# Kernel optimization log

Hardware: AMD Instinct MI355X
Metric: run time of the kernel (lower is better)

The kernel has to match this reference:

```python
import jax, jax.numpy as jnp
import numpy as np

B, N, IN_CH = 4, 8192, 4
K = 16
W0, W1, W2 = 64, 128, 256
NUM_CLASSES = 3


def setup_inputs() -> dict:
    key = jax.random.key(0)
    ks = jax.random.split(key, 16)

    def lin(kw, kb, fan_in, fan_out):
        bound = 1.0 / np.sqrt(fan_in)
        w = jax.random.uniform(kw, (fan_in, fan_out), jnp.float32, -bound, bound)
        b = jax.random.uniform(kb, (fan_out,), jnp.float32, -bound, bound)
        return w, b

    x = jax.random.normal(ks[0], (B, N, IN_CH), jnp.float32)
    stem_w, stem_b = lin(ks[1], ks[2], IN_CH, W0)
    b1_w, b1_b = lin(ks[3], ks[4], 2 * W0 + 3, W1)
    b2_w, b2_b = lin(ks[5], ks[6], 2 * W1 + 3, W2)
    glob_w, glob_b = lin(ks[7], ks[8], W2, W2)
    head1_w, head1_b = lin(ks[9], ks[10], 2 * W2, W2)
    head2_w, head2_b = lin(ks[11], ks[12], W2, NUM_CLASSES)
    return {
        'x': x,
        'hmix_a': jnp.float32(1.0), 'hmix_b': jnp.float32(1.0), 'hmix_c': jnp.float32(0.0),
        'stem_w': stem_w, 'stem_b': stem_b,
        'b1_w': b1_w, 'b1_b': b1_b,
        'b2_w': b2_w, 'b2_b': b2_b,
        'glob_w': glob_w, 'glob_b': glob_b,
        'head1_w': head1_w, 'head1_b': head1_b,
        'head2_w': head2_w, 'head2_b': head2_b,
        'thresh': jnp.float32(0.15), 'sharp': jnp.float32(10.0), 'scale': jnp.float32(0.5),
    }


def _knn_idx(coords, k):
    # coords: [B,N,3] -> idx of k nearest neighbors (incl. self), no grad.
    c = jax.lax.stop_gradient(coords)
    xx = jnp.sum(c * c, axis=-1, keepdims=True)            # [B,N,1]
    dist = xx + jnp.swapaxes(xx, 1, 2) - 2.0 * jnp.einsum('bnc,bmc->bnm', c, c)
    dist = jnp.maximum(dist, 0.0)
    _, idx = jax.lax.top_k(-dist, k)                       # smallest distances
    return idx                                             # [B,N,k]


def _local_agg(coords, feat, idx, w, b):
    # gather-concat-MLP-maxpool, faithful to LocalAggBlock (pool='max')
    bidx = jnp.arange(coords.shape[0])[:, None, None]
    nb_f = feat[bidx, idx]                                 # [B,N,k,C]
    nb_p = coords[bidx, idx]                               # [B,N,k,3]
    fi = feat[:, :, None, :]
    pi = coords[:, :, None, :]
    h = jnp.concatenate(
        [jnp.broadcast_to(fi, nb_f.shape), nb_f - fi, nb_p - pi], axis=-1)
    h = jax.nn.relu(jnp.einsum('bnkd,do->bnko', h, w) + b)
    return jnp.max(h, axis=2)                              # [B,N,out]


def reference(x, hmix_a, hmix_b, hmix_c, stem_w, stem_b, b1_w, b1_b,
              b2_w, b2_b, glob_w, glob_b, head1_w, head1_b,
              head2_w, head2_b, thresh, sharp, scale):
    # HeightMixer: z_eff = a*z + b*hag + c
    z_eff = hmix_a * x[..., 2] + hmix_b * x[..., 3] + hmix_c
    coords = jnp.stack([x[..., 0], x[..., 1], z_eff], axis=-1)  # [B,N,3]

    f = jax.nn.relu(x @ stem_w + stem_b)                   # stem: [B,N,64]

    # both blocks use the same coords -> same KNN graph; compute once
    idx = _knn_idx(coords, K)
    f = _local_agg(coords, f, idx, b1_w, b1_b)             # [B,N,128]
    f = _local_agg(coords, f, idx, b2_w, b2_b)             # [B,N,256]

    g = jnp.max(f, axis=1)                                 # [B,256]
    g = jax.nn.relu(g @ glob_w + glob_b)
    g = jnp.broadcast_to(g[:, None, :], f.shape)           # [B,N,256]

    h = jnp.concatenate([f, g], axis=-1)                   # [B,N,512]
    h = jax.nn.relu(h @ head1_w + head1_b)
    logits = h @ head2_w + head2_b                         # [B,N,3]

    # HeightPriorBias on class 0
    hag = x[..., 3]
    bias = scale * jax.nn.sigmoid(sharp * (thresh - hag))
    logits = logits.at[..., 0].add(bias)
    return logits
```

## Files before the change

kernel.cpp:

```cpp
#include <hip/hip_runtime.h>
#include <math.h>

typedef unsigned long long u64;
typedef unsigned int u32;
typedef _Float16 h8v __attribute__((ext_vector_type(8)));
typedef float    f4v __attribute__((ext_vector_type(4)));
typedef float    f2v __attribute__((ext_vector_type(2)));

#define MFMA16(a,b,c) __builtin_amdgcn_mfma_f32_16x16x32_f16(a, b, c, 0, 0, 0)

#define B_ 4
#define N_ 8192
#define K_ 16
#define W0_ 64
#define W1_ 128
#define W2_ 256
#define X0_ 96
#define X1_ 160
#define QAD_ 32
#define CAP_ 128

__global__ __launch_bounds__(256) void prep_kernel(
    const float* __restrict__ x,
    const float* __restrict__ stem_w, const float* __restrict__ stem_b,
    const float* __restrict__ hmix_a, const float* __restrict__ hmix_b,
    const float* __restrict__ hmix_c,
    float* __restrict__ coords4, _Float16* __restrict__ fx0,
    _Float16* __restrict__ fx1,
    const float* __restrict__ b1_w, const float* __restrict__ b2_w,
    const float* __restrict__ h1w,
    _Float16* __restrict__ w1m, _Float16* __restrict__ w1d,
    _Float16* __restrict__ w2m, _Float16* __restrict__ w2d,
    _Float16* __restrict__ h1wT,
    _Float16* __restrict__ qa, _Float16* __restrict__ cbq,
    float* __restrict__ part) {
  const int bi = blockIdx.x;
  const int tid = threadIdx.x;
  const int PB = (B_*N_)/4;
  if (bi < PB) {
    const int p = bi * 4 + (tid >> 6);
    const int o = tid & 63;
    const float x0 = x[p*4+0], x1 = x[p*4+1], x2 = x[p*4+2], x3 = x[p*4+3];
    const float z = hmix_a[0]*x2 + hmix_b[0]*x3 + hmix_c[0];
    float acc = stem_b[o] + x0*stem_w[0*W0_+o] + x1*stem_w[1*W0_+o]
              + x2*stem_w[2*W0_+o] + x3*stem_w[3*W0_+o];
    fx0[p*X0_+o] = (_Float16)fmaxf(acc, 0.f);
    if (o < 32) {
      const float tv = (o==0) ? x0 : (o==1) ? x1 : (o==2) ? z : 0.f;
      fx0[p*X0_+W0_+o] = (_Float16)tv;
      fx1[(size_t)p*X1_+W1_+o] = (_Float16)tv;
    }
    if (o == 0) {
      const float xx = x0*x0 + x1*x1 + z*z;
      ((float4*)coords4)[p] = make_float4(x0, x1, z, xx);
    } else if (o == 1) {
      const _Float16 hx = (_Float16)x0, hy = (_Float16)x1, hz = (_Float16)z;
      const _Float16 lx = (_Float16)(x0 - (float)hx);
      const _Float16 ly = (_Float16)(x1 - (float)hy);
      const _Float16 lz = (_Float16)(z  - (float)hz);
      const _Float16 one = (_Float16)1.f, Z = (_Float16)0.f;
      h8v a0 = {hx, hy, hz, lx, ly, lz, hx, hy};
      h8v a1 = {hz, lx, ly, lz, one, one, Z, Z};
      h8v zr = {Z,Z,Z,Z,Z,Z,Z,Z};
      *(h8v*)(qa + (size_t)p*QAD_)      = a0;
      *(h8v*)(qa + (size_t)p*QAD_ + 8)  = a1;
      *(h8v*)(qa + (size_t)p*QAD_ + 16) = zr;
      *(h8v*)(qa + (size_t)p*QAD_ + 24) = zr;
    } else if (o == 2) {
      const _Float16 hx = (_Float16)x0, hy = (_Float16)x1, hz = (_Float16)z;
      const _Float16 lx = (_Float16)(x0 - (float)hx);
      const _Float16 ly = (_Float16)(x1 - (float)hy);
      const _Float16 lz = (_Float16)(z  - (float)hz);
      const float xx = x0*x0 + x1*x1 + z*z;
      const _Float16 xh = (_Float16)xx;
      const _Float16 xl = (_Float16)(xx - (float)xh);
      const _Float16 nhx = (_Float16)(-2.f*(float)hx);
      const _Float16 nhy = (_Float16)(-2.f*(float)hy);
      const _Float16 nhz = (_Float16)(-2.f*(float)hz);
      const _Float16 nlx = (_Float16)(-2.f*(float)lx);
      const _Float16 nly = (_Float16)(-2.f*(float)ly);
      const _Float16 nlz = (_Float16)(-2.f*(float)lz);
      const _Float16 Z = (_Float16)0.f;
      h8v b0 = {nhx, nhy, nhz, nlx, nly, nlz, nlx, nly};
      h8v b1 = {nlz, nhx, nhy, nhz, xh, xl, Z, Z};
      h8v zr = {Z,Z,Z,Z,Z,Z,Z,Z};
      *(h8v*)(cbq + (size_t)p*QAD_)      = b0;
      *(h8v*)(cbq + (size_t)p*QAD_ + 8)  = b1;
      *(h8v*)(cbq + (size_t)p*QAD_ + 16) = zr;
      *(h8v*)(cbq + (size_t)p*QAD_ + 24) = zr;
    }
  } else if (bi < PB + W1_) {
    const int o = bi - PB, c = tid;
    if (c < X0_) {
      float mv = 0.f, dv = 0.f;
      if (c < W0_)        { const float wm = b1_w[(W0_+c)*W1_+o]; mv = wm; dv = b1_w[c*W1_+o] - wm; }
      else if (c < W0_+3) { const float wp = b1_w[(2*W0_+(c-W0_))*W1_+o]; mv = wp; dv = -wp; }
      w1m[o*X0_+c] = (_Float16)mv;
      w1d[o*X0_+c] = (_Float16)dv;
    }
  } else if (bi < PB + W1_ + W2_) {
    const int o = bi - PB - W1_, c = tid;
    if (c < X1_) {
      float mv = 0.f, dv = 0.f;
      if (c < W1_)        { const float wm = b2_w[(W1_+c)*W2_+o]; mv = wm; dv = b2_w[c*W2_+o] - wm; }
      else if (c < W1_+3) { const float wp = b2_w[(2*W1_+(c-W1_))*W2_+o]; mv = wp; dv = -wp; }
      w2m[o*X1_+c] = (_Float16)mv;
      w2d[o*X1_+c] = (_Float16)dv;
    }
  } else if (bi < PB + W1_ + 2*W2_) {
    const int o = bi - PB - W1_ - W2_;
    for (int c = tid; c < 512; c += 256)
      h1wT[(size_t)o*512 + c] = (_Float16)h1w[(size_t)c*256 + o];
  } else {
    ((float4*)part)[tid] = make_float4(0.f, 0.f, 0.f, 0.f);
  }
}

#define DPP_MIN(v, ctrl)                                                        \
  { const int _t = __builtin_amdgcn_update_dpp(0, __float_as_int(v),            \
      ctrl, 0xF, 0xF, false);                                                   \
    v = fminf(v, __int_as_float(_t)); }

__device__ __forceinline__ float sixteenth_of_minima(float v) {
  float th = 0.f;
#pragma unroll
  for (int r = 0; r < 16; ++r) {
    float w = v;
    DPP_MIN(w, 0x111); DPP_MIN(w, 0x112); DPP_MIN(w, 0x114); DPP_MIN(w, 0x118);
    DPP_MIN(w, 0x142); DPP_MIN(w, 0x143);
    const float mv = __int_as_float(
        __builtin_amdgcn_readlane(__float_as_int(w), 63));
    th = mv;
    v = (v == mv) ? INFINITY : v;
  }
  return th;
}

#define KNN_DIST2(dA, dB)                                                       \
  const f2v cjx = {cj.x, cj.x}, cjy = {cj.y, cj.y},                             \
            cjz = {cj.z, cj.z}, cjw = {cj.w, cj.w};                             \
  f2v tA = cAx * cjx;                                                           \
  tA = __builtin_elementwise_fma(cAy, cjy, tA);                                 \
  tA = __builtin_elementwise_fma(cAz, cjz, tA);                                 \
  const f2v dA = __builtin_elementwise_fma(tA, m2, cAw + cjw);                  \
  f2v tB = cBx * cjx;                                                           \
  tB = __builtin_elementwise_fma(cBy, cjy, tB);                                 \
  tB = __builtin_elementwise_fma(cBz, cjz, tB);                                 \
  const f2v dB = __builtin_elementwise_fma(tB, m2, cBw + cjw);

__global__ __launch_bounds__(256, 4) void knn_kernel(
    const float* __restrict__ coords4, const _Float16* __restrict__ qa,
    const _Float16* __restrict__ cbq, int* __restrict__ knn_idx) {
  const int tid = threadIdx.x;
  const int wid = tid >> 6;
  const int lane = tid & 63;
  const int col = lane & 15, quad = lane >> 4;
  const int p0 = blockIdx.x * 16;
  const int bb = (p0 >> 13) << 13;

  __shared__ float s_Tp[16];
  __shared__ int   s_cnt[16];
  __shared__ float s_ld[16][CAP_];
  __shared__ int   s_li[16][CAP_];
  if (tid < 16) s_cnt[tid] = 0;

  const float4* cb = ((const float4*)coords4) + bb;
  const int q0 = p0 + wid * 4;
  const float4 c0 = ((const float4*)coords4)[q0+0];
  const float4 c1 = ((const float4*)coords4)[q0+1];
  const float4 c2 = ((const float4*)coords4)[q0+2];
  const float4 c3 = ((const float4*)coords4)[q0+3];
  const f2v m2 = {-2.f, -2.f};
  const f2v cAx = {c0.x, c1.x}, cAy = {c0.y, c1.y}, cAz = {c0.z, c1.z}, cAw = {c0.w, c1.w};
  const f2v cBx = {c2.x, c3.x}, cBy = {c2.y, c3.y}, cBz = {c2.z, c3.z}, cBw = {c2.w, c3.w};

  float lm0 = INFINITY, lm1 = INFINITY, lm2 = INFINITY, lm3 = INFINITY;
  for (int it = 0; it < 64; ++it) {
    const float4 cj = cb[it*64 + lane];
    KNN_DIST2(dA, dB)
    lm0 = fminf(lm0, fmaxf(dA[0], 0.f));
    lm1 = fminf(lm1, fmaxf(dA[1], 0.f));
    lm2 = fminf(lm2, fmaxf(dB[0], 0.f));
    lm3 = fminf(lm3, fmaxf(dB[1], 0.f));
  }
  const float Th0 = sixteenth_of_minima(lm0);
  const float Th1 = sixteenth_of_minima(lm1);
  const float Th2 = sixteenth_of_minima(lm2);
  const float Th3 = sixteenth_of_minima(lm3);
  if (lane == 0) {
    s_Tp[wid*4+0] = Th0 - c0.w + (1e-3f + 1e-5f*c0.w);
    s_Tp[wid*4+1] = Th1 - c1.w + (1e-3f + 1e-5f*c1.w);
    s_Tp[wid*4+2] = Th2 - c2.w + (1e-3f + 1e-5f*c2.w);
    s_Tp[wid*4+3] = Th3 - c3.w + (1e-3f + 1e-5f*c3.w);
  }
  __syncthreads();

  const float Tq0 = s_Tp[quad*4+0], Tq1 = s_Tp[quad*4+1],
              Tq2 = s_Tp[quad*4+2], Tq3 = s_Tp[quad*4+3];
  const h8v afrag = *(const h8v*)(qa + (size_t)(p0 + col)*QAD_ + quad*8);
  const int cb0 = wid * 2048;
  const _Float16* cbp = cbq + (size_t)(bb + cb0 + col)*QAD_ + quad*8;

  h8v bcur = *(const h8v*)cbp;
#pragma unroll 2
  for (int t = 0; t < 128; ++t) {
    const int nx = ((t < 127) ? (t+1) : 0) * 16 * QAD_;
    const h8v bnxt = *(const h8v*)(cbp + nx);
    f4v acc = {0.f, 0.f, 0.f, 0.f};
    acc = MFMA16(afrag, bcur, acc);
    const int cidx = cb0 + t*16 + col;
    if (acc[0] < Tq0) { const int pos = atomicAdd(&s_cnt[quad*4+0], 1);
      if (pos < CAP_) { s_ld[quad*4+0][pos] = acc[0]; s_li[quad*4+0][pos] = cidx; } }
    if (acc[1] < Tq1) { const int pos = atomicAdd(&s_cnt[quad*4+1], 1);
      if (pos < CAP_) { s_ld[quad*4+1][pos] = acc[1]; s_li[quad*4+1][pos] = cidx; } }
    if (acc[2] < Tq2) { const int pos = atomicAdd(&s_cnt[quad*4+2], 1);
      if (pos < CAP_) { s_ld[quad*4+2][pos] = acc[2]; s_li[quad*4+2][pos] = cidx; } }
    if (acc[3] < Tq3) { const int pos = atomicAdd(&s_cnt[quad*4+3], 1);
      if (pos < CAP_) { s_ld[quad*4+3][pos] = acc[3]; s_li[quad*4+3][pos] = cidx; } }
    bcur = bnxt;
  }
  __syncthreads();

  for (int qq = 0; qq < 4; ++qq) {
    const int q = wid*4 + qq;
    const int cnt = s_cnt[q];
    const int L = (cnt < CAP_) ? cnt : CAP_;
    float d0 = (lane      < L) ? s_ld[q][lane]      : INFINITY;
    float d1 = (lane + 64 < L) ? s_ld[q][lane + 64] : INFINITY;
    int   i0 = (lane      < L) ? s_li[q][lane]      : 0x7fffffff;
    int   i1 = (lane + 64 < L) ? s_li[q][lane + 64] : 0x7fffffff;
    int keep = 0;
    for (int r = 0; r < K_; ++r) {
      float dl = d0; int il = i0; bool s1 = false;
      if (d1 < dl || (d1 == dl && i1 < il)) { dl = d1; il = i1; s1 = true; }
      float w = dl;
      DPP_MIN(w, 0x111); DPP_MIN(w, 0x112); DPP_MIN(w, 0x114); DPP_MIN(w, 0x118);
      DPP_MIN(w, 0x142); DPP_MIN(w, 0x143);
      const float dmin = __int_as_float(
          __builtin_amdgcn_readlane(__float_as_int(w), 63));
      u64 m = __ballot(dl == dmin);
      int bi = 0x7fffffff, bl = 0;
      do {
        const int s = (int)__ffsll((unsigned long long)m) - 1; m &= m - 1;
        const int ii = __builtin_amdgcn_readlane(il, s);
        if (ii < bi) { bi = ii; bl = s; }
      } while (m);
      if (lane == bl) { if (s1) d1 = INFINITY; else d0 = INFINITY; }
      if (lane == r) keep = bi;
    }
    if (lane < K_) knn_idx[(size_t)(p0 + q)*K_ + lane] = keep;
  }
}

template<int KS, int NPASS, bool GMAX>
__global__ __launch_bounds__(256) void aggm_kernel(
    const _Float16* __restrict__ fx, const int* __restrict__ knn_idx,
    const _Float16* __restrict__ midT, const _Float16* __restrict__ difT,
    const float* __restrict__ bw,
    _Float16* __restrict__ fo, const int ostr, u32* __restrict__ part) {
  const int XD  = KS*32;
  const int XDP = XD + 8;
  const int CH  = KS*4;
  const int p0 = blockIdx.x * 16;
  const int bb = (p0 >> 13) << 13;
  const int tid = threadIdx.x;
  const int w = tid >> 6, lane = tid & 63, col = lane & 15, quad = lane >> 4;
  const int koff = quad * 8;

  __shared__ int s_idx[256];
  __shared__ _Float16 sA[2][64*(KS*32+8)];

  s_idx[tid] = knn_idx[p0*K_ + tid];

  f4v cacc[NPASS][2];
  {
    h8v Ao[KS];
    const _Float16* ap = fx + (size_t)(p0+col)*XD + koff;
#pragma unroll
    for (int kk = 0; kk < KS; ++kk) Ao[kk] = *(const h8v*)(ap + kk*32);
#pragma unroll
    for (int ps = 0; ps < NPASS; ++ps) {
      const int o0 = ps*128 + w*32;
      const _Float16* b0 = difT + (size_t)(o0 + col)*XD + koff;
      const _Float16* b1 = difT + (size_t)(o0 + 16 + col)*XD + koff;
      f4v c0 = {0.f,0.f,0.f,0.f}, c1 = {0.f,0.f,0.f,0.f};
#pragma unroll
      for (int kk = 0; kk < KS; ++kk) {
        c0 = MFMA16(Ao[kk], *(const h8v*)(b0 + kk*32), c0);
        c1 = MFMA16(Ao[kk], *(const h8v*)(b1 + kk*32), c1);
      }
      cacc[ps][0] = c0; cacc[ps][1] = c1;
    }
  }

  h8v Bf[NPASS][2][KS];
  float bias[NPASS][2];
#pragma unroll
  for (int ps = 0; ps < NPASS; ++ps) {
    const int o0 = ps*128 + w*32;
#pragma unroll
    for (int kk = 0; kk < KS; ++kk) {
      Bf[ps][0][kk] = *(const h8v*)(midT + (size_t)(o0 + col)*XD + kk*32 + koff);
      Bf[ps][1][kk] = *(const h8v*)(midT + (size_t)(o0 + 16 + col)*XD + kk*32 + koff);
    }
    bias[ps][0] = bw[o0 + col];
    bias[ps][1] = bw[o0 + 16 + col];
  }
  __syncthreads();

  for (int c = tid; c < 64*CH; c += 256) {
    const int r = c / CH, o = c - r*CH;
    *(uint4*)&sA[0][r*XDP + o*8] =
        *(const uint4*)(fx + (size_t)(bb + s_idx[((r&15)<<4) + (r>>4)])*XD + o*8);
  }
  __syncthreads();

  f4v M[NPASS][2];
#pragma unroll
  for (int ps = 0; ps < NPASS; ++ps) {
    M[ps][0] = (f4v){-INFINITY,-INFINITY,-INFINITY,-INFINITY};
    M[ps][1] = (f4v){-INFINITY,-INFINITY,-INFINITY,-INFINITY};
  }

  for (int s = 0; s < 4; ++s) {
    const int buf = s & 1;
    if (s < 3) {
      for (int c = tid; c < 64*CH; c += 256) {
        const int r = c / CH, o = c - r*CH;
        *(uint4*)&sA[buf^1][r*XDP + o*8] =
            *(const uint4*)(fx + (size_t)(bb + s_idx[((r&15)<<4) + 4*s+4 + (r>>4)])*XD + o*8);
      }
    }
#pragma unroll
    for (int half = 0; half < 4; ++half) {
      h8v Ac[KS];
      const _Float16* ap = &sA[buf][(half*16 + col)*XDP + koff];
#pragma unroll
      for (int kk = 0; kk < KS; ++kk) Ac[kk] = *(const h8v*)(ap + kk*32);
#pragma unroll
      for (int ps = 0; ps < NPASS; ++ps) {
        f4v d0 = {0.f,0.f,0.f,0.f}, d1 = {0.f,0.f,0.f,0.f};
#pragma unroll
        for (int kk = 0; kk < KS; ++kk) {
          d0 = MFMA16(Ac[kk], Bf[ps][0][kk], d0);
          d1 = MFMA16(Ac[kk], Bf[ps][1][kk], d1);
        }
#pragma unroll
        for (int e = 0; e < 4; ++e) {
          M[ps][0][e] = fmaxf(M[ps][0][e], d0[e]);
          M[ps][1][e] = fmaxf(M[ps][1][e], d1[e]);
        }
      }
    }
    if (s < 3) __syncthreads();
  }

  const int prow = p0 + (quad << 2);
  const int bq = p0 >> 13;
#pragma unroll
  for (int ps = 0; ps < NPASS; ++ps) {
    const int o0 = ps*128 + w*32;
    const int oa = o0 + col, ob = oa + 16;
    float v0[4], v1[4];
#pragma unroll
    for (int reg = 0; reg < 4; ++reg) {
      v0[reg] = fmaxf(M[ps][0][reg] + cacc[ps][0][reg] + bias[ps][0], 0.f);
      v1[reg] = fmaxf(M[ps][1][reg] + cacc[ps][1][reg] + bias[ps][1], 0.f);
      fo[(size_t)(prow+reg)*ostr + oa] = (_Float16)v0[reg];
      fo[(size_t)(prow+reg)*ostr + ob] = (_Float16)v1[reg];
    }
    if (GMAX) {
      float bm0 = fmaxf(fmaxf(v0[0], v0[1]), fmaxf(v0[2], v0[3]));
      float bm1 = fmaxf(fmaxf(v1[0], v1[1]), fmaxf(v1[2], v1[3]));
      bm0 = fmaxf(bm0, __shfl_xor(bm0, 16, 64));
      bm0 = fmaxf(bm0, __shfl_xor(bm0, 32, 64));
      bm1 = fmaxf(bm1, __shfl_xor(bm1, 16, 64));
      bm1 = fmaxf(bm1, __shfl_xor(bm1, 32, 64));
      if (quad == 0) {
        atomicMax(part + bq*W2_ + oa, __float_as_uint(bm0));
        atomicMax(part + bq*W2_ + ob, __float_as_uint(bm1));
      }
    }
  }
}

__global__ __launch_bounds__(256) void gfc_kernel(
    const float* __restrict__ part, const float* __restrict__ gw,
    const float* __restrict__ gb, _Float16* __restrict__ g2h) {
  const int b = blockIdx.x;
  const int o = threadIdx.x;
  __shared__ float s_g[W2_];
  s_g[o] = part[b*W2_ + o];
  __syncthreads();
  float acc = gb[o];
  for (int d = 0; d < W2_; ++d) acc += s_g[d]*gw[d*W2_ + o];
  g2h[b*W2_ + o] = (_Float16)fmaxf(acc, 0.f);
}

__global__ __launch_bounds__(256) void headm_kernel(
    const _Float16* __restrict__ f2h, const _Float16* __restrict__ g2h,
    const _Float16* __restrict__ h1wT, const float* __restrict__ h1b,
    const float* __restrict__ h2w, const float* __restrict__ h2b,
    const float* __restrict__ x,
    const float* __restrict__ thresh, const float* __restrict__ sharp,
    const float* __restrict__ scale,
    float* __restrict__ out) {
  const int p0 = blockIdx.x * 32;
  const int b = p0 >> 13;
  const int tid = threadIdx.x;
  const int w = tid >> 6, lane = tid & 63, col = lane & 15, quad = lane >> 4;

  __shared__ _Float16 sA[32*520];
  __shared__ float    sh[32*260];

  for (int t = tid; t < 32*32; t += 256) {
    const int r = t >> 5, cc = (t & 31) * 8;
    *(uint4*)&sA[r*520 + cc] = *(const uint4*)&f2h[(size_t)(p0+r)*W2_ + cc];
  }
  for (int t = tid; t < 32*32; t += 256) {
    const int r = t >> 5, cc = (t & 31) * 8;
    *(uint4*)&sA[r*520 + 256 + cc] = *(const uint4*)&g2h[b*W2_ + cc];
  }
  __syncthreads();

  f4v acc[2][4];
#pragma unroll
  for (int r = 0; r < 2; ++r)
#pragma unroll
    for (int t = 0; t < 4; ++t) acc[r][t] = (f4v){0.f,0.f,0.f,0.f};

  for (int kk = 0; kk < 16; ++kk) {
    const h8v a0 = *(const h8v*)&sA[col*520 + kk*32 + quad*8];
    const h8v a1 = *(const h8v*)&sA[(16+col)*520 + kk*32 + quad*8];
#pragma unroll
    for (int t = 0; t < 4; ++t) {
      const h8v bt = *(const h8v*)&h1wT[(size_t)(w*64 + t*16 + col)*512 + kk*32 + quad*8];
      acc[0][t] = MFMA16(a0, bt, acc[0][t]);
      acc[1][t] = MFMA16(a1, bt, acc[1][t]);
    }
  }
#pragma unroll
  for (int r = 0; r < 2; ++r)
#pragma unroll
    for (int t = 0; t < 4; ++t) {
      const int o = w*64 + t*16 + col;
      const float bv = h1b[o];
#pragma unroll
      for (int reg = 0; reg < 4; ++reg)
        sh[(r*16 + quad*4 + reg)*260 + o] = fmaxf(acc[r][t][reg] + bv, 0.f);
    }
  __syncthreads();

  if (tid < 96) {
    const int pp = tid / 3, c = tid % 3;
    float s = h2b[c];
    for (int d = 0; d < 256; ++d) s += sh[pp*260 + d] * h2w[d*3 + c];
    if (c == 0) {
      const float hag = x[(size_t)(p0+pp)*4 + 3];
      s += scale[0] / (1.f + expf(-sharp[0]*(thresh[0] - hag)));
    }
    out[(size_t)(p0+pp)*3 + c] = s;
  }
}

extern "C" void kernel_launch(void* const* d_in, const int* in_sizes, int n_in,
                              void* d_out, int out_size, void* d_ws, size_t ws_size,
                              hipStream_t stream) {
  const float* x       = (const float*)d_in[0];
  const float* hmix_a  = (const float*)d_in[1];
  const float* hmix_b  = (const float*)d_in[2];
  const float* hmix_c  = (const float*)d_in[3];
  const float* stem_w  = (const float*)d_in[4];
  const float* stem_b  = (const float*)d_in[5];
  const float* b1_w    = (const float*)d_in[6];
  const float* b1_b    = (const float*)d_in[7];
  const float* b2_w    = (const float*)d_in[8];
  const float* b2_b    = (const float*)d_in[9];
  const float* glob_w  = (const float*)d_in[10];
  const float* glob_b  = (const float*)d_in[11];
  const float* head1_w = (const float*)d_in[12];
  const float* head1_b = (const float*)d_in[13];
  const float* head2_w = (const float*)d_in[14];
  const float* head2_b = (const float*)d_in[15];
  const float* thresh  = (const float*)d_in[16];
  const float* sharp   = (const float*)d_in[17];
  const float* scale   = (const float*)d_in[18];
  float* out = (float*)d_out;

  char* base = (char*)d_ws;
  float*     coords4 = (float*)    (base + 0);
  int*       idxb    = (int*)      (base + 524288);
  _Float16*  fx0     = (_Float16*) (base + 2621440);
  _Float16*  fx1     = (_Float16*) (base + 8912896);
  _Float16*  f2h     = (_Float16*) (base + 19398656);
  _Float16*  qa      = (_Float16*) (base + 19398656);
  _Float16*  cbq     = (_Float16*) (base + 21495808);
  _Float16*  w1m     = (_Float16*) (base + 36175872);
  _Float16*  w1d     = (_Float16*) (base + 36200448);
  _Float16*  w2m     = (_Float16*) (base + 36225024);
  _Float16*  w2d     = (_Float16*) (base + 36306944);
  _Float16*  h1wT    = (_Float16*) (base + 36388864);
  float*     part    = (float*)    (base + 36651008);
  _Float16*  g2h     = (_Float16*) (base + 36782080);
  const int NP = B_ * N_;

  prep_kernel<<<NP/4 + W1_ + 2*W2_ + 1, 256, 0, stream>>>(
      x, stem_w, stem_b, hmix_a, hmix_b, hmix_c, coords4, fx0, fx1,
      b1_w, b2_w, head1_w, w1m, w1d, w2m, w2d, h1wT, qa, cbq, part);
  knn_kernel<<<NP/16, 256, 0, stream>>>(coords4, qa, cbq, idxb);
  aggm_kernel<3, 1, false><<<NP/16, 256, 0, stream>>>(
      fx0, idxb, w1m, w1d, b1_b, fx1, X1_, (u32*)0);
  aggm_kernel<5, 2, true><<<NP/16, 256, 0, stream>>>(
      fx1, idxb, w2m, w2d, b2_b, f2h, W2_, (u32*)part);
  gfc_kernel<<<B_, 256, 0, stream>>>(part, glob_w, glob_b, g2h);
  headm_kernel<<<NP/32, 256, 0, stream>>>(f2h, g2h, h1wT, head1_b, head2_w, head2_b,
                                          x, thresh, sharp, scale, out);
}
```

Measured before the change: 394.6 us.

## Switch KNN distance pass to 32x32x16 MFMA with 32-query blocks

The KNN candidate-distance loop now uses the 32x32x16 f16 MFMA instead of 16x16x32, processing 32 queries per 512-thread block. The padded query and candidate rows shrink from 32 to 16 halves, since the extra K was all zeros. This halves the per-point fragment traffic and the number of MFMA issues per candidate. The cost is a larger accumulator per lane (16 thresholds and 16 compare/atomic branches), more shared memory, and a different block occupancy.

```diff
diff --git a/kernel.cpp b/kernel.cpp
--- a/kernel.cpp
+++ b/kernel.cpp
@@ -5,9 +5,11 @@
 typedef unsigned int u32;
 typedef _Float16 h8v __attribute__((ext_vector_type(8)));
 typedef float    f4v __attribute__((ext_vector_type(4)));
+typedef float    f16v __attribute__((ext_vector_type(16)));
 typedef float    f2v __attribute__((ext_vector_type(2)));
 
 #define MFMA16(a,b,c) __builtin_amdgcn_mfma_f32_16x16x32_f16(a, b, c, 0, 0, 0)
+#define MFMA32(a,b,c) __builtin_amdgcn_mfma_f32_32x32x16_f16(a, b, c, 0, 0, 0)
 
 #define B_ 4
 #define N_ 8192
@@ -17,7 +19,7 @@
 #define W2_ 256
 #define X0_ 96
 #define X1_ 160
-#define QAD_ 32
+#define QAD_ 16
 #define CAP_ 128
 
 __global__ __launch_bounds__(256) void prep_kernel(
@@ -61,11 +63,8 @@
       const _Float16 one = (_Float16)1.f, Z = (_Float16)0.f;
       h8v a0 = {hx, hy, hz, lx, ly, lz, hx, hy};
       h8v a1 = {hz, lx, ly, lz, one, one, Z, Z};
-      h8v zr = {Z,Z,Z,Z,Z,Z,Z,Z};
       *(h8v*)(qa + (size_t)p*QAD_)      = a0;
       *(h8v*)(qa + (size_t)p*QAD_ + 8)  = a1;
-      *(h8v*)(qa + (size_t)p*QAD_ + 16) = zr;
-      *(h8v*)(qa + (size_t)p*QAD_ + 24) = zr;
     } else if (o == 2) {
       const _Float16 hx = (_Float16)x0, hy = (_Float16)x1, hz = (_Float16)z;
       const _Float16 lx = (_Float16)(x0 - (float)hx);
@@ -83,11 +82,8 @@
       const _Float16 Z = (_Float16)0.f;
       h8v b0 = {nhx, nhy, nhz, nlx, nly, nlz, nlx, nly};
       h8v b1 = {nlz, nhx, nhy, nhz, xh, xl, Z, Z};
-      h8v zr = {Z,Z,Z,Z,Z,Z,Z,Z};
       *(h8v*)(cbq + (size_t)p*QAD_)      = b0;
       *(h8v*)(cbq + (size_t)p*QAD_ + 8)  = b1;
-      *(h8v*)(cbq + (size_t)p*QAD_ + 16) = zr;
-      *(h8v*)(cbq + (size_t)p*QAD_ + 24) = zr;
     }
   } else if (bi < PB + W1_) {
     const int o = bi - PB, c = tid;
@@ -148,21 +144,21 @@
   tB = __builtin_elementwise_fma(cBz, cjz, tB);                                 \
   const f2v dB = __builtin_elementwise_fma(tB, m2, cBw + cjw);
 
-__global__ __launch_bounds__(256, 4) void knn_kernel(
+__global__ __launch_bounds__(512) void knn_kernel(
     const float* __restrict__ coords4, const _Float16* __restrict__ qa,
     const _Float16* __restrict__ cbq, int* __restrict__ knn_idx) {
   const int tid = threadIdx.x;
   const int wid = tid >> 6;
   const int lane = tid & 63;
-  const int col = lane & 15, quad = lane >> 4;
-  const int p0 = blockIdx.x * 16;
+  const int p0 = blockIdx.x * 32;
   const int bb = (p0 >> 13) << 13;
 
-  __shared__ float s_Tp[16];
-  __shared__ int   s_cnt[16];
-  __shared__ float s_ld[16][CAP_];
-  __shared__ int   s_li[16][CAP_];
-  if (tid < 16) s_cnt[tid] = 0;
+  __shared__ float s_Tp[32];
+  __shared__ float s_Tpr[32];
+  __shared__ int   s_cnt[32];
+  __shared__ float s_ld[32][CAP_];
+  __shared__ int   s_li[32][CAP_];
+  if (tid < 32) s_cnt[tid] = 0;
 
   const float4* cb = ((const float4*)coords4) + bb;
   const int q0 = p0 + wid * 4;
@@ -194,29 +190,38 @@
     s_Tp[wid*4+3] = Th3 - c3.w + (1e-3f + 1e-5f*c3.w);
   }
   __syncthreads();
-
-  const float Tq0 = s_Tp[quad*4+0], Tq1 = s_Tp[quad*4+1],
-              Tq2 = s_Tp[quad*4+2], Tq3 = s_Tp[quad*4+3];
-  const h8v afrag = *(const h8v*)(qa + (size_t)(p0 + col)*QAD_ + quad*8);
-  const int cb0 = wid * 2048;
-  const _Float16* cbp = cbq + (size_t)(bb + cb0 + col)*QAD_ + quad*8;
+  if (tid < 32) {
+    const int h = tid >> 4, r = tid & 15;
+    s_Tpr[tid] = s_Tp[(r&3) + 8*(r>>2) + 4*h];
+  }
+  __syncthreads();
+
+  const int half = lane >> 5;
+  const int lrow = lane & 31;
+  float Tv[16];
+  *(f4v*)&Tv[0]  = *(const f4v*)&s_Tpr[half*16 + 0];
+  *(f4v*)&Tv[4]  = *(const f4v*)&s_Tpr[half*16 + 4];
+  *(f4v*)&Tv[8]  = *(const f4v*)&s_Tpr[half*16 + 8];
+  *(f4v*)&Tv[12] = *(const f4v*)&s_Tpr[half*16 + 12];
+  const h8v afrag = *(const h8v*)(qa + (size_t)(p0 + lrow)*QAD_ + half*8);
+  const int c0b = wid * 1024;
+  const _Float16* cbp = cbq + (size_t)(bb + c0b + lrow)*QAD_ + half*8;
+  const f16v zacc = (f16v)0.0f;
 
   h8v bcur = *(const h8v*)cbp;
 #pragma unroll 2
-  for (int t = 0; t < 128; ++t) {
-    const int nx = ((t < 127) ? (t+1) : 0) * 16 * QAD_;
-    const h8v bnxt = *(const h8v*)(cbp + nx);
-    f4v acc = {0.f, 0.f, 0.f, 0.f};
-    acc = MFMA16(afrag, bcur, acc);
-    const int cidx = cb0 + t*16 + col;
-    if (acc[0] < Tq0) { const int pos = atomicAdd(&s_cnt[quad*4+0], 1);
-      if (pos < CAP_) { s_ld[quad*4+0][pos] = acc[0]; s_li[quad*4+0][pos] = cidx; } }
-    if (acc[1] < Tq1) { const int pos = atomicAdd(&s_cnt[quad*4+1], 1);
-      if (pos < CAP_) { s_ld[quad*4+1][pos] = acc[1]; s_li[quad*4+1][pos] = cidx; } }
-    if (acc[2] < Tq2) { const int pos = atomicAdd(&s_cnt[quad*4+2], 1);
-      if (pos < CAP_) { s_ld[quad*4+2][pos] = acc[2]; s_li[quad*4+2][pos] = cidx; } }
-    if (acc[3] < Tq3) { const int pos = atomicAdd(&s_cnt[quad*4+3], 1);
-      if (pos < CAP_) { s_ld[quad*4+3][pos] = acc[3]; s_li[quad*4+3][pos] = cidx; } }
+  for (int t = 0; t < 32; ++t) {
+    const h8v bnxt = *(const h8v*)(cbp + (size_t)((t < 31) ? (t+1) : 0) * 32 * QAD_);
+    const f16v acc = MFMA32(afrag, bcur, zacc);
+    const int cidx = c0b + t*32 + lrow;
+#pragma unroll
+    for (int r = 0; r < 16; ++r) {
+      if (acc[r] < Tv[r]) {
+        const int q = (r&3) + 8*(r>>2) + 4*half;
+        const int pos = atomicAdd(&s_cnt[q], 1);
+        if (pos < CAP_) { s_ld[q][pos] = acc[r]; s_li[q][pos] = cidx; }
+      }
+    }
     bcur = bnxt;
   }
   __syncthreads();
@@ -494,7 +499,7 @@
   _Float16*  fx1     = (_Float16*) (base + 8912896);
   _Float16*  f2h     = (_Float16*) (base + 19398656);
   _Float16*  qa      = (_Float16*) (base + 19398656);
-  _Float16*  cbq     = (_Float16*) (base + 21495808);
+  _Float16*  cbq     = (_Float16*) (base + 20447232);
   _Float16*  w1m     = (_Float16*) (base + 36175872);
   _Float16*  w1d     = (_Float16*) (base + 36200448);
   _Float16*  w2m     = (_Float16*) (base + 36225024);
@@ -507,7 +512,7 @@
   prep_kernel<<<NP/4 + W1_ + 2*W2_ + 1, 256, 0, stream>>>(
       x, stem_w, stem_b, hmix_a, hmix_b, hmix_c, coords4, fx0, fx1,
       b1_w, b2_w, head1_w, w1m, w1d, w2m, w2d, h1wT, qa, cbq, part);
-  knn_kernel<<<NP/16, 256, 0, stream>>>(coords4, qa, cbq, idxb);
+  knn_kernel<<<NP/32, 512, 0, stream>>>(coords4, qa, cbq, idxb);
   aggm_kernel<3, 1, false><<<NP/16, 256, 0, stream>>>(
       fx0, idxb, w1m, w1d, b1_b, fx1, X1_, (u32*)0);
   aggm_kernel<5, 2, true><<<NP/16, 256, 0, stream>>>(
```

New measurement: 375.5 us. 1.05x faster.
